# Kernel optimization log

Measured on AMD Instinct MI355X. Metric: run time of the kernel, lower is better.

Reference implementation:

```python
import jax, jax.numpy as jnp
import numpy as np

N = 50000      # nodes
E = 800000     # edges (avg degree 16)
IN = 128       # input feature dim
D = 128        # embed dim (heads=1, concat)
SLOPE = 0.2    # GATv2Conv default negative_slope


def setup_inputs() -> dict:
    key = jax.random.key(0)
    ks = jax.random.split(key, 16)
    s_in = 1.0 / np.sqrt(IN)
    s_d = 1.0 / np.sqrt(D)
    inp = {
        "node_fts": jax.random.normal(ks[0], (N, IN), dtype=jnp.float32),
        "edge_index": jax.random.randint(ks[1], (2, E), 0, N, dtype=jnp.int64),
        # layer 1 (in_dim -> embed_dim)
        "Wl1": jax.random.normal(ks[2], (IN, D), dtype=jnp.float32) * s_in,
        "bl1": jnp.zeros((D,), dtype=jnp.float32),
        "Wr1": jax.random.normal(ks[3], (IN, D), dtype=jnp.float32) * s_in,
        "br1": jnp.zeros((D,), dtype=jnp.float32),
        "att1": jax.random.normal(ks[4], (D,), dtype=jnp.float32) * s_d,
        "bias1": jnp.zeros((D,), dtype=jnp.float32),
        # layer 2 (embed_dim -> embed_dim)
        "Wl2": jax.random.normal(ks[5], (D, D), dtype=jnp.float32) * s_d,
        "bl2": jnp.zeros((D,), dtype=jnp.float32),
        "Wr2": jax.random.normal(ks[6], (D, D), dtype=jnp.float32) * s_d,
        "br2": jnp.zeros((D,), dtype=jnp.float32),
        "att2": jax.random.normal(ks[7], (D,), dtype=jnp.float32) * s_d,
        "bias2": jnp.zeros((D,), dtype=jnp.float32),
    }
    return inp


def gatv2_layer(x, src, dst, Wl, bl, Wr, br, att, bias):
    # GATv2Conv (heads=1, share_weights=False):
    #   x_j (source message features) = lin_l(x), x_i (target) = lin_r(x)
    xl = x @ Wl + bl                                      # [N, D]
    xr = x @ Wr + br                                      # [N, D]
    e = jax.nn.leaky_relu(xl[src] + xr[dst], SLOPE)       # [E, D]
    logits = e @ att                                      # [E]
    # softmax over incoming edges of each target node
    m = jax.ops.segment_max(logits, dst, num_segments=N)  # [N], -inf for isolated
    m = jnp.where(jnp.isneginf(m), 0.0, m)
    a = jnp.exp(logits - m[dst])                          # [E]
    s = jax.ops.segment_sum(a, dst, num_segments=N)       # [N]
    a = a / jnp.maximum(s[dst], 1e-16)
    out = jax.ops.segment_sum(a[:, None] * xl[src], dst, num_segments=N)  # [N, D]
    return out + bias


def reference(node_fts, edge_index,
              Wl1, bl1, Wr1, br1, att1, bias1,
              Wl2, bl2, Wr2, br2, att2, bias2):
    src, dst = edge_index[0], edge_index[1]
    x = jax.nn.relu(gatv2_layer(node_fts, src, dst, Wl1, bl1, Wr1, br1, att1, bias1))
    x = jax.nn.relu(gatv2_layer(x, src, dst, Wl2, bl2, Wr2, br2, att2, bias2))
    return x
```

## Files before the change

### kernel.cpp

```cpp
#include <hip/hip_runtime.h>
#include <hip/hip_bf16.h>
#include <hip/hip_fp16.h>

#define N_NODES 50000
#define N_EDGES 800000
#define DIM 128
#define NGROUPS (N_NODES / 16)
#define LROW2 132
#define KBUCKET 196
#define BCAP 5120
#define EPB 2000

typedef __attribute__((ext_vector_type(8))) _Float16 hfrag8;
typedef __attribute__((ext_vector_type(4))) float f32x4;
typedef _Float16 h2 __attribute__((ext_vector_type(2)));

__device__ __forceinline__ h2 u2h(uint u){ union{uint u; h2 h;} c; c.u = u; return c.h; }


__global__ __launch_bounds__(256) void bucket_scatter_k(
    const int* __restrict__ src, const int* __restrict__ dst,
    int* __restrict__ bucket_cnt, uint* __restrict__ bucketdata)
{
  __shared__ int cnt[KBUCKET], base[KBUCKET], cur[KBUCKET];
  int tid = threadIdx.x;
  for (int t = tid; t < KBUCKET; t += 256) { cnt[t] = 0; cur[t] = 0; }
  __syncthreads();
  int e0 = blockIdx.x * EPB;
  for (int i = tid; i < EPB; i += 256)
    atomicAdd(&cnt[dst[e0 + i] >> 8], 1);
  __syncthreads();
  for (int t = tid; t < KBUCKET; t += 256)
    base[t] = atomicAdd(&bucket_cnt[t], cnt[t]);
  __syncthreads();
  for (int i = tid; i < EPB; i += 256) {
    int s = src[e0 + i], d = dst[e0 + i];
    int b = d >> 8;
    int r = atomicAdd(&cur[b], 1);
    bucketdata[(size_t)b * BCAP + base[b] + r] = ((uint)s << 8) | (uint)(d & 255);
  }
}

__global__ __launch_bounds__(256) void bucket_csr_k(
    const int* __restrict__ bucket_cnt, const uint* __restrict__ bucketdata,
    int* __restrict__ row_start, int* __restrict__ csr_src)
{
  __shared__ int hist[256], cur[256];
  __shared__ int wsumA[4], wsumB[4];
  int b = blockIdx.x, tid = threadIdx.x;
  int lane = tid & 63, w = tid >> 6;
  int vv = (tid < b) ? bucket_cnt[tid] : 0;
  #pragma unroll
  for (int off = 32; off > 0; off >>= 1) vv += __shfl_xor(vv, off, 64);
  if (lane == 0) wsumA[w] = vv;
  hist[tid] = 0;
  __syncthreads();
  int base_csr = wsumA[0] + wsumA[1] + wsumA[2] + wsumA[3];
  int cnt = bucket_cnt[b];
  int node0 = b << 8;
  const uint* bd = bucketdata + (size_t)b * BCAP;
  for (int i = tid; i < cnt; i += 256)
    atomicAdd(&hist[bd[i] & 255], 1);
  __syncthreads();
  int v = hist[tid];
  int inc = v;
  #pragma unroll
  for (int off = 1; off < 64; off <<= 1) {
    int y = __shfl_up(inc, off, 64);
    if (lane >= off) inc += y;
  }
  if (lane == 63) wsumB[w] = inc;
  __syncthreads();
  int wpre = 0;
  #pragma unroll
  for (int i = 0; i < 4; i++) if (i < w) wpre += wsumB[i];
  int excl = wpre + inc - v;
  int node = node0 + tid;
  if (node < N_NODES) row_start[node] = base_csr + excl;
  if (b == 0 && tid == 0) row_start[N_NODES] = N_EDGES;
  cur[tid] = excl;
  __syncthreads();
  for (int i = tid; i < cnt; i += 256) {
    uint p = bd[i];
    int r = atomicAdd(&cur[p & 255], 1);
    csr_src[base_csr + r] = (int)(p >> 8);
  }
}

__global__ __launch_bounds__(64) void prep_w(
    const float* __restrict__ Wl1, const float* __restrict__ Wr1,
    const float* __restrict__ Wl2, const float* __restrict__ Wr2,
    _Float16* __restrict__ wb, int* __restrict__ bucket_cnt)
{
  int bid = blockIdx.x;
  if (bid == 0) {
    for (int t = threadIdx.x; t < KBUCKET; t += 64) bucket_cnt[t] = 0;
  }
  int layer = bid >> 6, rest = bid & 63;
  int C = rest >> 4, g = rest & 15;
  int lane = threadIdx.x;
  int m = lane & 15, q = lane >> 4;
  int dim = g*16 + m;
  const float* W = layer ? (dim < 128 ? Wl2 : Wr2) : (dim < 128 ? Wl1 : Wr1);
  int dcol = dim & 127;
  _Float16 h[8];
  #pragma unroll
  for (int j = 0; j < 8; j++) {
    int k = C*32 + q*8 + j;
    h[j] = (_Float16)W[(size_t)k*DIM + dcol];
  }
  size_t off = ((size_t)bid*64 + lane)*8;
  *(hfrag8*)(wb + off) = *(hfrag8*)h;
}

template<typename TIN>
__global__ __launch_bounds__(256) void gemm_mfma(
    const TIN* __restrict__ x,
    const _Float16* __restrict__ wb,
    const float* __restrict__ bl, const float* __restrict__ br,
    __half* __restrict__ xlh, __half* __restrict__ xrh)
{
  __shared__ float lds[4][16*LROW2];
  int wv = threadIdx.x >> 6, lane = threadIdx.x & 63;
  int G = blockIdx.x * 4 + wv;
  if (G >= NGROUPS) return;

  int m = lane & 15, q = lane >> 4;
  const TIN* xrow = x + (size_t)(G*16 + m)*DIM + q*8;

  f32x4 acc[16];
  #pragma unroll
  for (int g = 0; g < 16; g++) acc[g] = (f32x4)(0.f);

  #pragma unroll 1
  for (int C = 0; C < 4; C++) {
    hfrag8 ah;
    if constexpr (sizeof(TIN) == 4) {
      float v[8];
      *(float4*)(v)     = *(const float4*)((const float*)xrow + C*32);
      *(float4*)(v + 4) = *(const float4*)((const float*)xrow + C*32 + 4);
      _Float16 hh[8];
      #pragma unroll
      for (int j = 0; j < 8; j++) hh[j] = (_Float16)v[j];
      ah = *(hfrag8*)hh;
    } else {
      ah = *(const hfrag8*)((const _Float16*)xrow + C*32);
    }
    #pragma unroll
    for (int g = 0; g < 16; g++) {
      size_t boff = ((size_t)(C*16 + g)*64 + lane)*8;
      hfrag8 bh = *(const hfrag8*)(wb + boff);
      acc[g] = __builtin_amdgcn_mfma_f32_16x16x32_f16(ah, bh, acc[g], 0, 0, 0);
    }
  }

  float* wlds = lds[wv];
  int dcol = (lane & 31) * 4;
  int rowsel = lane >> 5;
  #pragma unroll
  for (int half = 0; half < 2; half++) {
    #pragma unroll
    for (int g = 0; g < 8; g++) {
      #pragma unroll
      for (int r = 0; r < 4; r++)
        wlds[(q*4 + r)*LROW2 + g*16 + m] = acc[half*8 + g][r];
    }
    const float* B = half ? br : bl;
    ushort* outh = half ? (ushort*)xrh : (ushort*)xlh;
    float4 bv = *(const float4*)(B + dcol);
    #pragma unroll
    for (int it = 0; it < 8; it++) {
      int i = it*2 + rowsel;
      float4 vv = *(const float4*)(wlds + i*LROW2 + dcol);
      int node = G*16 + i;
      __half2 h0 = __floats2half2_rn(vv.x + bv.x, vv.y + bv.y);
      __half2 h1 = __floats2half2_rn(vv.z + bv.z, vv.w + bv.w);
      uint2 pk = make_uint2(*(uint*)&h0, *(uint*)&h1);
      *(uint2*)(outh + (size_t)node*DIM + dcol) = pk;
    }
  }
}

template<int OUT>
__global__ __launch_bounds__(256) void gat_gather(
    const __half* __restrict__ xlh, const __half* __restrict__ xrh,
    const int* __restrict__ row_start, const int* __restrict__ csr_src,
    const float* __restrict__ att, const float* __restrict__ bias,
    float* __restrict__ outf, __half* __restrict__ outh)
{
  int wave = (blockIdx.x * 256 + threadIdx.x) >> 6;
  int lane = threadIdx.x & 63;
  int q4 = lane >> 4;
  int hl = lane & 15;
  int node = wave * 4 + q4;
  int r0 = row_start[node];
  int deg = row_start[node + 1] - r0;
  int last = r0 + deg - 1;

  uint4 rx = *(const uint4*)((const ushort*)xrh + (size_t)node*DIM + hl*8);
  h2 xr01 = u2h(rx.x), xr23 = u2h(rx.y), xr45 = u2h(rx.z), xr67 = u2h(rx.w);
  const float* ap = att + hl*8;
  float4 af0 = *(const float4*)(ap);
  float4 af1 = *(const float4*)(ap + 4);
  h2 a01 = {(_Float16)af0.x, (_Float16)af0.y};
  h2 a23 = {(_Float16)af0.z, (_Float16)af0.w};
  h2 a45 = {(_Float16)af1.x, (_Float16)af1.y};
  h2 a67 = {(_Float16)af1.z, (_Float16)af1.w};
  const h2 c02 = {(_Float16)0.2f, (_Float16)0.2f};

  float l = 0.f;
  float b0a=0,b1a=0,b2a=0,b3a=0,b4a=0,b5a=0,b6a=0,b7a=0;
  const ushort* xbase = (const ushort*)xlh + hl*8;

  for (int t = 0; t < deg; t += 8) {
    int idx[8];
    #pragma unroll
    for (int j = 0; j < 8; j++) {
      int rr = r0 + t + j;
      idx[j] = csr_src[rr <= last ? rr : last];
    }
    uint4 raw[8];
    #pragma unroll
    for (int j = 0; j < 8; j++)
      raw[j] = *(const uint4*)(xbase + (size_t)idx[j]*DIM);
    #pragma unroll
    for (int j = 0; j < 8; j++) {
      h2 v01 = u2h(raw[j].x), v23 = u2h(raw[j].y);
      h2 v45 = u2h(raw[j].z), v67 = u2h(raw[j].w);
      h2 s01 = v01 + xr01, s23 = v23 + xr23;
      h2 s45 = v45 + xr45, s67 = v67 + xr67;
      s01 = __builtin_elementwise_max(s01, s01 * c02);
      s23 = __builtin_elementwise_max(s23, s23 * c02);
      s45 = __builtin_elementwise_max(s45, s45 * c02);
      s67 = __builtin_elementwise_max(s67, s67 * c02);
      float p = __builtin_amdgcn_fdot2(s01, a01, 0.f, false);
      p = __builtin_amdgcn_fdot2(s23, a23, p, false);
      p = __builtin_amdgcn_fdot2(s45, a45, p, false);
      p = __builtin_amdgcn_fdot2(s67, a67, p, false);
      #pragma unroll
      for (int o = 1; o <= 8; o <<= 1) p += __shfl_xor(p, o, 64);
      float w = (t + j < deg) ? __expf(p) : 0.f;
      l += w;
      b0a = fmaf(w, (float)v01.x, b0a); b1a = fmaf(w, (float)v01.y, b1a);
      b2a = fmaf(w, (float)v23.x, b2a); b3a = fmaf(w, (float)v23.y, b3a);
      b4a = fmaf(w, (float)v45.x, b4a); b5a = fmaf(w, (float)v45.y, b5a);
      b6a = fmaf(w, (float)v67.x, b6a); b7a = fmaf(w, (float)v67.y, b7a);
    }
  }

  float inv = 1.f / fmaxf(l, 1e-16f);
  const float* bp = bias + hl*8;
  float4 c0 = *(const float4*)(bp);
  float4 c1 = *(const float4*)(bp + 4);
  float4 o0, o1;
  o0.x = fmaxf(fmaf(b0a, inv, c0.x), 0.f);
  o0.y = fmaxf(fmaf(b1a, inv, c0.y), 0.f);
  o0.z = fmaxf(fmaf(b2a, inv, c0.z), 0.f);
  o0.w = fmaxf(fmaf(b3a, inv, c0.w), 0.f);
  o1.x = fmaxf(fmaf(b4a, inv, c1.x), 0.f);
  o1.y = fmaxf(fmaf(b5a, inv, c1.y), 0.f);
  o1.z = fmaxf(fmaf(b6a, inv, c1.z), 0.f);
  o1.w = fmaxf(fmaf(b7a, inv, c1.w), 0.f);
  if (OUT == 0) {
    float* op = outf + (size_t)node*DIM + hl*8;
    *(float4*)(op)     = o0;
    *(float4*)(op + 4) = o1;
  } else {
    __half2 h0 = __floats2half2_rn(o0.x, o0.y);
    __half2 h1 = __floats2half2_rn(o0.z, o0.w);
    __half2 h2v = __floats2half2_rn(o1.x, o1.y);
    __half2 h3 = __floats2half2_rn(o1.z, o1.w);
    uint4 pk = make_uint4(*(uint*)&h0, *(uint*)&h1, *(uint*)&h2v, *(uint*)&h3);
    *(uint4*)((ushort*)outh + (size_t)node*DIM + hl*8) = pk;
  }
}

extern "C" void kernel_launch(void* const* d_in, const int* in_sizes, int n_in,
                              void* d_out, int out_size, void* d_ws, size_t ws_size,
                              hipStream_t stream)
{
  const float* node_fts = (const float*)d_in[0];
  const int*  edge_index = (const int*)d_in[1];
  const float* Wl1 = (const float*)d_in[2];
  const float* bl1 = (const float*)d_in[3];
  const float* Wr1 = (const float*)d_in[4];
  const float* br1 = (const float*)d_in[5];
  const float* att1 = (const float*)d_in[6];
  const float* bias1 = (const float*)d_in[7];
  const float* Wl2 = (const float*)d_in[8];
  const float* bl2 = (const float*)d_in[9];
  const float* Wr2 = (const float*)d_in[10];
  const float* br2 = (const float*)d_in[11];
  const float* att2 = (const float*)d_in[12];
  const float* bias2 = (const float*)d_in[13];
  const int* src = edge_index;
  const int* dst = edge_index + N_EDGES;

  char* ws = (char*)d_ws;
  __half* xlh = (__half*)ws;               ws += (size_t)N_NODES*DIM*2;
  __half* xrh = (__half*)ws;               ws += (size_t)N_NODES*DIM*2;
  __half* hh  = (__half*)ws;               ws += (size_t)N_NODES*DIM*2;
  _Float16* wb = (_Float16*)ws;            ws += 2*4*16*64*8*2;
  int* row_start   = (int*)ws;             ws += (N_NODES+1)*4;
  int* csr_src     = (int*)ws;             ws += (size_t)N_EDGES*4;
  int* bucket_cnt  = (int*)ws;             ws += KBUCKET*4;
  uint* bucketdata = (uint*)ws;            ws += (size_t)KBUCKET*BCAP*4;

  const int W_LAYER = 4*16*64*8;

  int gemm_blocks = (NGROUPS + 3) / 4;
  int gather_blocks = N_NODES / 16;

  prep_w<<<128, 64, 0, stream>>>(Wl1, Wr1, Wl2, Wr2, wb, bucket_cnt);

  bucket_scatter_k<<<N_EDGES/EPB, 256, 0, stream>>>(src, dst, bucket_cnt, bucketdata);
  bucket_csr_k<<<KBUCKET, 256, 0, stream>>>(bucket_cnt, bucketdata, row_start, csr_src);

  gemm_mfma<float><<<gemm_blocks, 256, 0, stream>>>(node_fts, wb, bl1, br1, xlh, xrh);
  gat_gather<1><<<gather_blocks, 256, 0, stream>>>(xlh, xrh, row_start, csr_src,
                                                   att1, bias1, nullptr, hh);
  gemm_mfma<_Float16><<<gemm_blocks, 256, 0, stream>>>((const _Float16*)hh,
                                             wb + W_LAYER, bl2, br2, xlh, xrh);
  gat_gather<0><<<gather_blocks, 256, 0, stream>>>(xlh, xrh, row_start, csr_src,
                                                   att2, bias2, (float*)d_out, nullptr);
}
```

Measured before the change: 248.2 us.

## Fuse layer-1 gather with layer-2 GEMM and merge CSR build into GEMM1

Merges the CSR-building kernel into the first GEMM launch as extra independent blocks. It also fuses the layer-1 attention gather with the layer-2 projection GEMM through shared memory, so the intermediate hidden features never round-trip through global memory. The bucket scatter now keeps dst values in registers instead of loading them twice. Together these remove two kernel launches and a full N×128 half write/read. The fused kernel does less GEMM work per block and uses a swizzled LDS layout, which may lower GEMM efficiency and occupancy.

```diff
diff --git a/kernel.cpp b/kernel.cpp
--- a/kernel.cpp
+++ b/kernel.cpp
@@ -27,63 +27,26 @@
   for (int t = tid; t < KBUCKET; t += 256) { cnt[t] = 0; cur[t] = 0; }
   __syncthreads();
   int e0 = blockIdx.x * EPB;
-  for (int i = tid; i < EPB; i += 256)
-    atomicAdd(&cnt[dst[e0 + i] >> 8], 1);
+  int dreg[8];
+  #pragma unroll
+  for (int it = 0; it < 8; it++) {
+    int i = it*256 + tid;
+    dreg[it] = (i < EPB) ? dst[e0 + i] : -1;
+    if (i < EPB) atomicAdd(&cnt[dreg[it] >> 8], 1);
+  }
   __syncthreads();
   for (int t = tid; t < KBUCKET; t += 256)
     base[t] = atomicAdd(&bucket_cnt[t], cnt[t]);
   __syncthreads();
-  for (int i = tid; i < EPB; i += 256) {
-    int s = src[e0 + i], d = dst[e0 + i];
-    int b = d >> 8;
-    int r = atomicAdd(&cur[b], 1);
-    bucketdata[(size_t)b * BCAP + base[b] + r] = ((uint)s << 8) | (uint)(d & 255);
-  }
-}
-
-__global__ __launch_bounds__(256) void bucket_csr_k(
-    const int* __restrict__ bucket_cnt, const uint* __restrict__ bucketdata,
-    int* __restrict__ row_start, int* __restrict__ csr_src)
-{
-  __shared__ int hist[256], cur[256];
-  __shared__ int wsumA[4], wsumB[4];
-  int b = blockIdx.x, tid = threadIdx.x;
-  int lane = tid & 63, w = tid >> 6;
-  int vv = (tid < b) ? bucket_cnt[tid] : 0;
-  #pragma unroll
-  for (int off = 32; off > 0; off >>= 1) vv += __shfl_xor(vv, off, 64);
-  if (lane == 0) wsumA[w] = vv;
-  hist[tid] = 0;
-  __syncthreads();
-  int base_csr = wsumA[0] + wsumA[1] + wsumA[2] + wsumA[3];
-  int cnt = bucket_cnt[b];
-  int node0 = b << 8;
-  const uint* bd = bucketdata + (size_t)b * BCAP;
-  for (int i = tid; i < cnt; i += 256)
-    atomicAdd(&hist[bd[i] & 255], 1);
-  __syncthreads();
-  int v = hist[tid];
-  int inc = v;
-  #pragma unroll
-  for (int off = 1; off < 64; off <<= 1) {
-    int y = __shfl_up(inc, off, 64);
-    if (lane >= off) inc += y;
-  }
-  if (lane == 63) wsumB[w] = inc;
-  __syncthreads();
-  int wpre = 0;
-  #pragma unroll
-  for (int i = 0; i < 4; i++) if (i < w) wpre += wsumB[i];
-  int excl = wpre + inc - v;
-  int node = node0 + tid;
-  if (node < N_NODES) row_start[node] = base_csr + excl;
-  if (b == 0 && tid == 0) row_start[N_NODES] = N_EDGES;
-  cur[tid] = excl;
-  __syncthreads();
-  for (int i = tid; i < cnt; i += 256) {
-    uint p = bd[i];
-    int r = atomicAdd(&cur[p & 255], 1);
-    csr_src[base_csr + r] = (int)(p >> 8);
+  #pragma unroll
+  for (int it = 0; it < 8; it++) {
+    int i = it*256 + tid;
+    if (i < EPB) {
+      int s = src[e0 + i], d = dreg[it];
+      int b = d >> 8;
+      int r = atomicAdd(&cur[b], 1);
+      bucketdata[(size_t)b * BCAP + base[b] + r] = ((uint)s << 8) | (uint)(d & 255);
+    }
   }
 }
 
@@ -113,20 +76,66 @@
   *(hfrag8*)(wb + off) = *(hfrag8*)h;
 }
 
-template<typename TIN>
-__global__ __launch_bounds__(256) void gemm_mfma(
-    const TIN* __restrict__ x,
-    const _Float16* __restrict__ wb,
+__global__ __launch_bounds__(256) void gemm1_csr_k(
+    const float* __restrict__ x, const _Float16* __restrict__ wb,
     const float* __restrict__ bl, const float* __restrict__ br,
-    __half* __restrict__ xlh, __half* __restrict__ xrh)
+    __half* __restrict__ xlh, __half* __restrict__ xrh,
+    const int* __restrict__ bucket_cnt, const uint* __restrict__ bucketdata,
+    int* __restrict__ row_start, int* __restrict__ csr_src)
 {
   __shared__ float lds[4][16*LROW2];
-  int wv = threadIdx.x >> 6, lane = threadIdx.x & 63;
-  int G = blockIdx.x * 4 + wv;
+  __shared__ int hist[256], cur[256];
+  __shared__ int wsumA[4], wsumB[4];
+  int tid = threadIdx.x;
+
+  if (blockIdx.x < KBUCKET) {
+    int b = blockIdx.x;
+    int lane = tid & 63, w = tid >> 6;
+    int vv = (tid < b) ? bucket_cnt[tid] : 0;
+    #pragma unroll
+    for (int off = 32; off > 0; off >>= 1) vv += __shfl_xor(vv, off, 64);
+    if (lane == 0) wsumA[w] = vv;
+    hist[tid] = 0;
+    __syncthreads();
+    int base_csr = wsumA[0] + wsumA[1] + wsumA[2] + wsumA[3];
+    int cnt = bucket_cnt[b];
+    int node0 = b << 8;
+    const uint* bd = bucketdata + (size_t)b * BCAP;
+    for (int i = tid; i < cnt; i += 256)
+      atomicAdd(&hist[bd[i] & 255], 1);
+    __syncthreads();
+    int v = hist[tid];
+    int inc = v;
+    #pragma unroll
+    for (int off = 1; off < 64; off <<= 1) {
+      int y = __shfl_up(inc, off, 64);
+      if (lane >= off) inc += y;
+    }
+    if (lane == 63) wsumB[w] = inc;
+    __syncthreads();
+    int wpre = 0;
+    #pragma unroll
+    for (int i = 0; i < 4; i++) if (i < w) wpre += wsumB[i];
+    int excl = wpre + inc - v;
+    int node = node0 + tid;
+    if (node < N_NODES) row_start[node] = base_csr + excl;
+    if (b == 0 && tid == 0) row_start[N_NODES] = N_EDGES;
+    cur[tid] = excl;
+    __syncthreads();
+    for (int i = tid; i < cnt; i += 256) {
+      uint p = bd[i];
+      int r = atomicAdd(&cur[p & 255], 1);
+      csr_src[base_csr + r] = (int)(p >> 8);
+    }
+    return;
+  }
+
+  int wv = tid >> 6, lane = tid & 63;
+  int G = (blockIdx.x - KBUCKET) * 4 + wv;
   if (G >= NGROUPS) return;
 
   int m = lane & 15, q = lane >> 4;
-  const TIN* xrow = x + (size_t)(G*16 + m)*DIM + q*8;
+  const float* xrow = x + (size_t)(G*16 + m)*DIM + q*8;
 
   f32x4 acc[16];
   #pragma unroll
@@ -134,18 +143,13 @@
 
   #pragma unroll 1
   for (int C = 0; C < 4; C++) {
-    hfrag8 ah;
-    if constexpr (sizeof(TIN) == 4) {
-      float v[8];
-      *(float4*)(v)     = *(const float4*)((const float*)xrow + C*32);
-      *(float4*)(v + 4) = *(const float4*)((const float*)xrow + C*32 + 4);
-      _Float16 hh[8];
-      #pragma unroll
-      for (int j = 0; j < 8; j++) hh[j] = (_Float16)v[j];
-      ah = *(hfrag8*)hh;
-    } else {
-      ah = *(const hfrag8*)((const _Float16*)xrow + C*32);
-    }
+    float v[8];
+    *(float4*)(v)     = *(const float4*)(xrow + C*32);
+    *(float4*)(v + 4) = *(const float4*)(xrow + C*32 + 4);
+    _Float16 hh[8];
+    #pragma unroll
+    for (int j = 0; j < 8; j++) hh[j] = (_Float16)v[j];
+    hfrag8 ah = *(hfrag8*)hh;
     #pragma unroll
     for (int g = 0; g < 16; g++) {
       size_t boff = ((size_t)(C*16 + g)*64 + lane)*8;
@@ -181,18 +185,13 @@
   }
 }
 
-template<int OUT>
-__global__ __launch_bounds__(256) void gat_gather(
+__device__ __forceinline__ void gather_core(
+    int node, int hl,
     const __half* __restrict__ xlh, const __half* __restrict__ xrh,
     const int* __restrict__ row_start, const int* __restrict__ csr_src,
     const float* __restrict__ att, const float* __restrict__ bias,
-    float* __restrict__ outf, __half* __restrict__ outh)
-{
-  int wave = (blockIdx.x * 256 + threadIdx.x) >> 6;
-  int lane = threadIdx.x & 63;
-  int q4 = lane >> 4;
-  int hl = lane & 15;
-  int node = wave * 4 + q4;
+    float4& o0, float4& o1)
+{
   int r0 = row_start[node];
   int deg = row_start[node + 1] - r0;
   int last = r0 + deg - 1;
@@ -252,7 +251,6 @@
   const float* bp = bias + hl*8;
   float4 c0 = *(const float4*)(bp);
   float4 c1 = *(const float4*)(bp + 4);
-  float4 o0, o1;
   o0.x = fmaxf(fmaf(b0a, inv, c0.x), 0.f);
   o0.y = fmaxf(fmaf(b1a, inv, c0.y), 0.f);
   o0.z = fmaxf(fmaf(b2a, inv, c0.z), 0.f);
@@ -261,18 +259,91 @@
   o1.y = fmaxf(fmaf(b5a, inv, c1.y), 0.f);
   o1.z = fmaxf(fmaf(b6a, inv, c1.z), 0.f);
   o1.w = fmaxf(fmaf(b7a, inv, c1.w), 0.f);
-  if (OUT == 0) {
-    float* op = outf + (size_t)node*DIM + hl*8;
-    *(float4*)(op)     = o0;
-    *(float4*)(op + 4) = o1;
-  } else {
-    __half2 h0 = __floats2half2_rn(o0.x, o0.y);
-    __half2 h1 = __floats2half2_rn(o0.z, o0.w);
-    __half2 h2v = __floats2half2_rn(o1.x, o1.y);
-    __half2 h3 = __floats2half2_rn(o1.z, o1.w);
-    uint4 pk = make_uint4(*(uint*)&h0, *(uint*)&h1, *(uint*)&h2v, *(uint*)&h3);
-    *(uint4*)((ushort*)outh + (size_t)node*DIM + hl*8) = pk;
-  }
+}
+
+__global__ __launch_bounds__(256) void fused_g1_gemm2_k(
+    const __half* __restrict__ xlh, const __half* __restrict__ xrh,
+    const int* __restrict__ row_start, const int* __restrict__ csr_src,
+    const float* __restrict__ att, const float* __restrict__ bias,
+    const _Float16* __restrict__ wb2,
+    const float* __restrict__ bl2, const float* __restrict__ br2,
+    __half* __restrict__ xlh2, __half* __restrict__ xrh2)
+{
+  __shared__ ushort xs[16*128];
+  __shared__ ushort outs[16*256];
+  int tid = threadIdx.x;
+  int wv = tid >> 6, lane = tid & 63;
+  int q4 = lane >> 4, hl = lane & 15;
+  int nl = wv*4 + q4;
+  int base = blockIdx.x * 16;
+
+  float4 o0, o1;
+  gather_core(base + nl, hl, xlh, xrh, row_start, csr_src, att, bias, o0, o1);
+  __half2 p0 = __floats2half2_rn(o0.x, o0.y);
+  __half2 p1 = __floats2half2_rn(o0.z, o0.w);
+  __half2 p2 = __floats2half2_rn(o1.x, o1.y);
+  __half2 p3 = __floats2half2_rn(o1.z, o1.w);
+  uint4 pk = make_uint4(*(uint*)&p0, *(uint*)&p1, *(uint*)&p2, *(uint*)&p3);
+  *(uint4*)((char*)xs + nl*256 + ((hl*16) ^ ((nl&7)<<4))) = pk;
+  __syncthreads();
+
+  int m = lane & 15, q = lane >> 4;
+  f32x4 acc[4];
+  #pragma unroll
+  for (int g = 0; g < 4; g++) acc[g] = (f32x4)(0.f);
+  #pragma unroll
+  for (int C = 0; C < 4; C++) {
+    hfrag8 ah = *(const hfrag8*)((const char*)xs + m*256 + ((C*64 + q*16) ^ ((m&7)<<4)));
+    #pragma unroll
+    for (int g = 0; g < 4; g++) {
+      int gg = wv*4 + g;
+      size_t boff = ((size_t)(C*16 + gg)*64 + lane)*8;
+      hfrag8 bh = *(const hfrag8*)(wb2 + boff);
+      acc[g] = __builtin_amdgcn_mfma_f32_16x16x32_f16(ah, bh, acc[g], 0, 0, 0);
+    }
+  }
+  #pragma unroll
+  for (int g = 0; g < 4; g++) {
+    int gg = wv*4 + g;
+    int dim = gg*16 + m;
+    float bv = (gg < 8) ? bl2[dim] : br2[dim - 128];
+    #pragma unroll
+    for (int r = 0; r < 4; r++) {
+      int row = q*4 + r;
+      __half hv = __float2half_rn(acc[g][r] + bv);
+      outs[row*256 + gg*16 + m] = *(ushort*)&hv;
+    }
+  }
+  __syncthreads();
+  #pragma unroll
+  for (int p = 0; p < 2; p++) {
+    int c = p*256 + tid;
+    int row = c >> 5, off = c & 31;
+    uint4 v = *(const uint4*)((const char*)outs + row*512 + off*16);
+    int nodeo = base + row;
+    int d0 = off*8;
+    ushort* dstp = (d0 < 128) ? ((ushort*)xlh2 + (size_t)nodeo*DIM + d0)
+                              : ((ushort*)xrh2 + (size_t)nodeo*DIM + (d0 - 128));
+    *(uint4*)dstp = v;
+  }
+}
+
+__global__ __launch_bounds__(256) void gat_gather2(
+    const __half* __restrict__ xlh, const __half* __restrict__ xrh,
+    const int* __restrict__ row_start, const int* __restrict__ csr_src,
+    const float* __restrict__ att, const float* __restrict__ bias,
+    float* __restrict__ outf)
+{
+  int wave = (blockIdx.x * 256 + threadIdx.x) >> 6;
+  int lane = threadIdx.x & 63;
+  int q4 = lane >> 4;
+  int hl = lane & 15;
+  int node = wave * 4 + q4;
+  float4 o0, o1;
+  gather_core(node, hl, xlh, xrh, row_start, csr_src, att, bias, o0, o1);
+  float* op = outf + (size_t)node*DIM + hl*8;
+  *(float4*)(op)     = o0;
+  *(float4*)(op + 4) = o1;
 }
 
 extern "C" void kernel_launch(void* const* d_in, const int* in_sizes, int n_in,
@@ -299,7 +370,8 @@
   char* ws = (char*)d_ws;
   __half* xlh = (__half*)ws;               ws += (size_t)N_NODES*DIM*2;
   __half* xrh = (__half*)ws;               ws += (size_t)N_NODES*DIM*2;
-  __half* hh  = (__half*)ws;               ws += (size_t)N_NODES*DIM*2;
+  __half* xlh2 = (__half*)ws;              ws += (size_t)N_NODES*DIM*2;
+  __half* xrh2 = (__half*)ws;              ws += (size_t)N_NODES*DIM*2;
   _Float16* wb = (_Float16*)ws;            ws += 2*4*16*64*8*2;
   int* row_start   = (int*)ws;             ws += (N_NODES+1)*4;
   int* csr_src     = (int*)ws;             ws += (size_t)N_EDGES*4;
@@ -312,15 +384,13 @@
   int gather_blocks = N_NODES / 16;
 
   prep_w<<<128, 64, 0, stream>>>(Wl1, Wr1, Wl2, Wr2, wb, bucket_cnt);
-
   bucket_scatter_k<<<N_EDGES/EPB, 256, 0, stream>>>(src, dst, bucket_cnt, bucketdata);
-  bucket_csr_k<<<KBUCKET, 256, 0, stream>>>(bucket_cnt, bucketdata, row_start, csr_src);
-
-  gemm_mfma<float><<<gemm_blocks, 256, 0, stream>>>(node_fts, wb, bl1, br1, xlh, xrh);
-  gat_gather<1><<<gather_blocks, 256, 0, stream>>>(xlh, xrh, row_start, csr_src,
-                                                   att1, bias1, nullptr, hh);
-  gemm_mfma<_Float16><<<gemm_blocks, 256, 0, stream>>>((const _Float16*)hh,
-                                             wb + W_LAYER, bl2, br2, xlh, xrh);
-  gat_gather<0><<<gather_blocks, 256, 0, stream>>>(xlh, xrh, row_start, csr_src,
-                                                   att2, bias2, (float*)d_out, nullptr);
-}
+  gemm1_csr_k<<<KBUCKET + gemm_blocks, 256, 0, stream>>>(
+      node_fts, wb, bl1, br1, xlh, xrh,
+      bucket_cnt, bucketdata, row_start, csr_src);
+  fused_g1_gemm2_k<<<NGROUPS, 256, 0, stream>>>(
+      xlh, xrh, row_start, csr_src, att1, bias1,
+      wb + W_LAYER, bl2, br2, xlh2, xrh2);
+  gat_gather2<<<gather_blocks, 256, 0, stream>>>(
+      xlh2, xrh2, row_start, csr_src, att2, bias2, (float*)d_out);
+}
```

After: 218.1 us. 12.1% less time.
